# Performance work log

Measured on AMD Instinct MI355X. Metric: run time of the kernel, lower is better.

The kernel has to match this reference:

```python
import jax, jax.numpy as jnp
import numpy as np

K = 3  # kernel_size

def setup_inputs() -> dict:
    key = jax.random.key(0)
    ks = jax.random.split(key, 7)
    B, C, H, W = 4, 128, 128, 128
    MID = int(C * 0.2)  # 25
    return {
        "x":  jax.random.normal(ks[0], (B, C, H, W), dtype=jnp.float32),
        "Ws": jax.random.normal(ks[1], (K * K, C), dtype=jnp.float32) * 0.1,
        "bs": jax.random.normal(ks[2], (K * K,), dtype=jnp.float32) * 0.1,
        "W1": jax.random.normal(ks[3], (MID, C), dtype=jnp.float32) * 0.1,
        "b1": jax.random.normal(ks[4], (MID,), dtype=jnp.float32) * 0.1,
        "W2": jax.random.normal(ks[5], (C * K * K, MID), dtype=jnp.float32) * 0.1,
        "b2": jax.random.normal(ks[6], (C * K * K,), dtype=jnp.float32) * 0.1,
    }

def reference(x, Ws, bs, W1, b1, W2, b2):
    b, c, h, w = x.shape
    k = K
    # channel branch: global avg pool -> 1x1 conv -> relu -> 1x1 conv -> sigmoid
    xm = x.mean(axis=(2, 3))                                   # [b, c]
    hid = jax.nn.relu(xm @ W1.T + b1)                          # [b, mid]
    channel_filter = jax.nn.sigmoid(hid @ W2.T + b2)           # [b, c*k*k]
    channel_filter = channel_filter.reshape(b, c, k * k, 1, 1)
    # spatial branch: 1x1 conv C -> k*k, sigmoid
    spatial_filter = jax.nn.sigmoid(
        jnp.einsum('bchw,oc->bohw', x, Ws) + bs[None, :, None, None]
    ).reshape(b, 1, k * k, h, w)
    filt = spatial_filter * channel_filter                     # [b, c, k*k, h, w]
    # unfold (k=3, pad=1, stride=1, dilation=1): stack 9 shifted views
    xp = jnp.pad(x, ((0, 0), (0, 0), (1, 1), (1, 1)))
    patches = jnp.stack(
        [xp[:, :, i:i + h, j:j + w] for i in range(k) for j in range(k)],
        axis=2,
    )  # [b, c, k*k, h, w] — matches nn.Unfold's (c, k*k) ordering
    return (patches * filt).sum(axis=2)                        # [b, c, h, w]
```

## Files before the change

kernel.cpp:

```cpp
#include <hip/hip_runtime.h>

#define B 4
#define C 128
#define H 128
#define W 128
#define HW (H * W)
#define KK 9
#define MID 25

#define WS_XM 0
#define WS_CH 1024
#define WS_S  8192

__global__ __launch_bounds__(256) void k_mean(
    const float* __restrict__ x, float* __restrict__ xm)
{
    const int c = blockIdx.x, b = blockIdx.y;
    const float4* plane = (const float4*)(x + ((size_t)b * C + c) * HW);
    float s = 0.0f;
#pragma unroll
    for (int i = 0; i < 16; ++i) {
        float4 v = plane[i * 256 + threadIdx.x];
        s += (v.x + v.y) + (v.z + v.w);
    }
#pragma unroll
    for (int off = 32; off > 0; off >>= 1) s += __shfl_down(s, off, 64);
    __shared__ float red[4];
    if ((threadIdx.x & 63) == 0) red[threadIdx.x >> 6] = s;
    __syncthreads();
    if (threadIdx.x == 0)
        xm[b * C + c] = ((red[0] + red[1]) + (red[2] + red[3])) * (1.0f / HW);
}

__global__ __launch_bounds__(256) void k_spatial(
    const float* __restrict__ x, const float* __restrict__ Ws,
    const float* __restrict__ bs, float* __restrict__ S)
{
    const int lane = threadIdx.x & 63;
    const int wave = threadIdx.x >> 6;
    const int b = blockIdx.y;
    const int p = blockIdx.x * 64 + lane;
    const float* xb = x + (size_t)b * C * HW + p;

    float acc[KK];
#pragma unroll
    for (int k = 0; k < KK; ++k) acc[k] = (wave == 0) ? bs[k] : 0.0f;

    const int cbase = wave * 32;
#pragma unroll
    for (int i = 0; i < 32; ++i) {
        const int c = cbase + i;
        float v = xb[(size_t)c * HW];
#pragma unroll
        for (int k = 0; k < KK; ++k)
            acc[k] = fmaf(v, Ws[k * C + c], acc[k]);
    }

    __shared__ float red[3 * KK * 64];
    if (wave > 0) {
#pragma unroll
        for (int k = 0; k < KK; ++k)
            red[((wave - 1) * KK + k) * 64 + lane] = acc[k];
    }
    __syncthreads();
    if (wave == 0) {
#pragma unroll
        for (int k = 0; k < KK; ++k) {
            float a = acc[k] + red[(0 * KK + k) * 64 + lane]
                             + red[(1 * KK + k) * 64 + lane]
                             + red[(2 * KK + k) * 64 + lane];
            S[((size_t)(b * KK + k)) * HW + p] = 1.0f / (1.0f + __expf(-a));
        }
    }
}

__global__ __launch_bounds__(512) void k_mlp(
    const float* __restrict__ xm, const float* __restrict__ W1,
    const float* __restrict__ b1, const float* __restrict__ W2,
    const float* __restrict__ b2, float* __restrict__ ch)
{
    __shared__ float xmean[B * C];
    __shared__ float hid[B * MID];
    const int tid = threadIdx.x;

    if (tid < B * C) xmean[tid] = xm[tid];
    __syncthreads();

    if (tid < B * MID) {
        const int b = tid / MID, m = tid % MID;
        float a = b1[m];
        for (int c = 0; c < C; ++c)
            a = fmaf(xmean[b * C + c], W1[m * C + c], a);
        hid[tid] = fmaxf(a, 0.0f);
    }
    __syncthreads();

    for (int idx = tid; idx < B * C * KK; idx += 512) {
        const int b = idx / (C * KK);
        const int o = idx % (C * KK);
        float a = b2[o];
#pragma unroll
        for (int m = 0; m < MID; ++m)
            a = fmaf(hid[b * MID + m], W2[o * MID + m], a);
        ch[idx] = 1.0f / (1.0f + __expf(-a));
    }
}

__global__ __launch_bounds__(256) void k_conv(
    const float* __restrict__ x, const float* __restrict__ S,
    const float* __restrict__ ch, float* __restrict__ out)
{
    const int tid = threadIdx.x;
    const int b = blockIdx.y;
    const int p = blockIdx.x * 256 + tid;
    const int h = p / W, w = p % W;

    float sv[KK];
    int off[KK];
    const float* Sb = S + (size_t)b * KK * HW + p;
#pragma unroll
    for (int k = 0; k < KK; ++k) {
        const int di = k / 3 - 1, dj = k % 3 - 1;
        const int hh = h + di, ww = w + dj;
        const bool valid = (hh >= 0) & (hh < H) & (ww >= 0) & (ww < W);
        const int hc = min(max(hh, 0), H - 1);
        const int wc = min(max(ww, 0), W - 1);
        off[k] = hc * W + wc;
        sv[k] = valid ? Sb[(size_t)k * HW] : 0.0f;
    }

    const int c0 = blockIdx.z * (C / 8);
    const float* xb = x + (size_t)b * C * HW;
    const float* chb = ch + b * C * KK;
    float* ob = out + (size_t)b * C * HW;

#pragma unroll 4
    for (int c = c0; c < c0 + C / 8; ++c) {
        const float* xc = xb + (size_t)c * HW;
        float acc = 0.0f;
#pragma unroll
        for (int k = 0; k < KK; ++k) {
            acc = fmaf(xc[off[k]], sv[k] * chb[c * KK + k], acc);
        }
        ob[(size_t)c * HW + p] = acc;
    }
}

extern "C" void kernel_launch(void* const* d_in, const int* in_sizes, int n_in,
                              void* d_out, int out_size, void* d_ws, size_t ws_size,
                              hipStream_t stream) {
    (void)in_sizes; (void)n_in; (void)out_size; (void)ws_size;
    const float* x  = (const float*)d_in[0];
    const float* Ws = (const float*)d_in[1];
    const float* bs = (const float*)d_in[2];
    const float* W1 = (const float*)d_in[3];
    const float* b1 = (const float*)d_in[4];
    const float* W2 = (const float*)d_in[5];
    const float* b2 = (const float*)d_in[6];
    float* out = (float*)d_out;
    float* ws  = (float*)d_ws;

    float* xm = ws + WS_XM;
    float* ch = ws + WS_CH;
    float* S  = ws + WS_S;

    k_mean<<<dim3(C, B), 256, 0, stream>>>(x, xm);
    k_spatial<<<dim3(HW / 64, B), 256, 0, stream>>>(x, Ws, bs, S);
    k_mlp<<<1, 512, 0, stream>>>(xm, W1, b1, W2, b2, ch);
    k_conv<<<dim3(HW / 256, B, 8), 256, 0, stream>>>(x, S, ch, out);
}
```

Baseline: 134.8 us.

## Fuse mean and spatial kernels, parallelize MLP, vectorize conv to four pixels per thread

Merges the mean-pool and spatial-filter kernels into one launch by giving them different block ranges, which removes one launch and lets both read x concurrently. The channel MLP is split across 18 blocks instead of running in one block. Each conv thread now computes four adjacent pixels with float4 loads and reuses each row between the shifted taps, so fewer scalar gathers are issued. The channel split doubles to 16 groups to keep enough blocks in flight. Every MLP block recomputes the hidden layer, and the float4 path assumes W is a multiple of 4.

```diff
diff --git a/kernel.cpp b/kernel.cpp
--- a/kernel.cpp
+++ b/kernel.cpp
@@ -8,37 +8,40 @@
 #define KK 9
 #define MID 25
 
+#define SPATIAL_BLKS (HW / 64)
+
 #define WS_XM 0
 #define WS_CH 1024
 #define WS_S  8192
 
-__global__ __launch_bounds__(256) void k_mean(
-    const float* __restrict__ x, float* __restrict__ xm)
+__global__ __launch_bounds__(256) void k_ms(
+    const float* __restrict__ x, const float* __restrict__ Ws,
+    const float* __restrict__ bs, float* __restrict__ xm,
+    float* __restrict__ S)
 {
-    const int c = blockIdx.x, b = blockIdx.y;
-    const float4* plane = (const float4*)(x + ((size_t)b * C + c) * HW);
-    float s = 0.0f;
+    __shared__ float red[3 * KK * 64];
+    const int b = blockIdx.y;
+
+    if (blockIdx.x >= SPATIAL_BLKS) {
+        const int c = blockIdx.x - SPATIAL_BLKS;
+        const float4* plane = (const float4*)(x + ((size_t)b * C + c) * HW);
+        float s = 0.0f;
 #pragma unroll
-    for (int i = 0; i < 16; ++i) {
-        float4 v = plane[i * 256 + threadIdx.x];
-        s += (v.x + v.y) + (v.z + v.w);
+        for (int i = 0; i < 16; ++i) {
+            float4 v = plane[i * 256 + threadIdx.x];
+            s += (v.x + v.y) + (v.z + v.w);
+        }
+#pragma unroll
+        for (int off = 32; off > 0; off >>= 1) s += __shfl_down(s, off, 64);
+        if ((threadIdx.x & 63) == 0) red[threadIdx.x >> 6] = s;
+        __syncthreads();
+        if (threadIdx.x == 0)
+            xm[b * C + c] = ((red[0] + red[1]) + (red[2] + red[3])) * (1.0f / HW);
+        return;
     }
-#pragma unroll
-    for (int off = 32; off > 0; off >>= 1) s += __shfl_down(s, off, 64);
-    __shared__ float red[4];
-    if ((threadIdx.x & 63) == 0) red[threadIdx.x >> 6] = s;
-    __syncthreads();
-    if (threadIdx.x == 0)
-        xm[b * C + c] = ((red[0] + red[1]) + (red[2] + red[3])) * (1.0f / HW);
-}
 
-__global__ __launch_bounds__(256) void k_spatial(
-    const float* __restrict__ x, const float* __restrict__ Ws,
-    const float* __restrict__ bs, float* __restrict__ S)
-{
     const int lane = threadIdx.x & 63;
     const int wave = threadIdx.x >> 6;
-    const int b = blockIdx.y;
     const int p = blockIdx.x * 64 + lane;
     const float* xb = x + (size_t)b * C * HW + p;
 
@@ -56,7 +59,6 @@
             acc[k] = fmaf(v, Ws[k * C + c], acc[k]);
     }
 
-    __shared__ float red[3 * KK * 64];
     if (wave > 0) {
 #pragma unroll
         for (int k = 0; k < KK; ++k)
@@ -74,7 +76,7 @@
     }
 }
 
-__global__ __launch_bounds__(512) void k_mlp(
+__global__ __launch_bounds__(256) void k_mlp(
     const float* __restrict__ xm, const float* __restrict__ W1,
     const float* __restrict__ b1, const float* __restrict__ W2,
     const float* __restrict__ b2, float* __restrict__ ch)
@@ -83,27 +85,27 @@
     __shared__ float hid[B * MID];
     const int tid = threadIdx.x;
 
-    if (tid < B * C) xmean[tid] = xm[tid];
+    for (int i = tid; i < B * C; i += 256) xmean[i] = xm[i];
     __syncthreads();
 
     if (tid < B * MID) {
         const int b = tid / MID, m = tid % MID;
         float a = b1[m];
+#pragma unroll 8
         for (int c = 0; c < C; ++c)
             a = fmaf(xmean[b * C + c], W1[m * C + c], a);
         hid[tid] = fmaxf(a, 0.0f);
     }
     __syncthreads();
 
-    for (int idx = tid; idx < B * C * KK; idx += 512) {
-        const int b = idx / (C * KK);
-        const int o = idx % (C * KK);
-        float a = b2[o];
+    const int idx = blockIdx.x * 256 + tid;
+    const int b = idx / (C * KK);
+    const int o = idx % (C * KK);
+    float a = b2[o];
 #pragma unroll
-        for (int m = 0; m < MID; ++m)
-            a = fmaf(hid[b * MID + m], W2[o * MID + m], a);
-        ch[idx] = 1.0f / (1.0f + __expf(-a));
-    }
+    for (int m = 0; m < MID; ++m)
+        a = fmaf(hid[b * MID + m], W2[o * MID + m], a);
+    ch[idx] = 1.0f / (1.0f + __expf(-a));
 }
 
 __global__ __launch_bounds__(256) void k_conv(
@@ -112,37 +114,59 @@
 {
     const int tid = threadIdx.x;
     const int b = blockIdx.y;
-    const int p = blockIdx.x * 256 + tid;
-    const int h = p / W, w = p % W;
+    const int p0 = (blockIdx.x * 256 + tid) * 4;
+    const int h = p0 >> 7;
+    const int w0 = p0 & (W - 1);
 
-    float sv[KK];
-    int off[KK];
-    const float* Sb = S + (size_t)b * KK * HW + p;
+    float4 sv[KK];
+    const float* Sb = S + (size_t)b * KK * HW + p0;
 #pragma unroll
     for (int k = 0; k < KK; ++k) {
         const int di = k / 3 - 1, dj = k % 3 - 1;
-        const int hh = h + di, ww = w + dj;
-        const bool valid = (hh >= 0) & (hh < H) & (ww >= 0) & (ww < W);
-        const int hc = min(max(hh, 0), H - 1);
-        const int wc = min(max(ww, 0), W - 1);
-        off[k] = hc * W + wc;
-        sv[k] = valid ? Sb[(size_t)k * HW] : 0.0f;
+        const int hh = h + di;
+        float4 s4 = *(const float4*)(Sb + (size_t)k * HW);
+        if (hh < 0 || hh >= H) s4 = make_float4(0.f, 0.f, 0.f, 0.f);
+        if (dj == -1 && w0 == 0)     s4.x = 0.f;
+        if (dj == +1 && w0 == W - 4) s4.w = 0.f;
+        sv[k] = s4;
     }
 
-    const int c0 = blockIdx.z * (C / 8);
+    const int r0 = max(h - 1, 0), r2 = min(h + 1, H - 1);
+    const int rowoff[3] = { r0 * W + w0, h * W + w0, r2 * W + w0 };
+    const int loff = (w0 > 0) ? -1 : 0;
+    const int roff = (w0 < W - 4) ? 4 : 0;
+
+    const int c0 = blockIdx.z * (C / 16);
     const float* xb = x + (size_t)b * C * HW;
     const float* chb = ch + b * C * KK;
-    float* ob = out + (size_t)b * C * HW;
+    float* ob = out + (size_t)b * C * HW + p0;
 
-#pragma unroll 4
-    for (int c = c0; c < c0 + C / 8; ++c) {
+    for (int c = c0; c < c0 + C / 16; ++c) {
         const float* xc = xb + (size_t)c * HW;
-        float acc = 0.0f;
+        float4 Cx[3];
+        float  Lw[3], Rx[3];
+#pragma unroll
+        for (int r = 0; r < 3; ++r) {
+            const float* bp = xc + rowoff[r];
+            Cx[r] = *(const float4*)bp;
+            Lw[r] = bp[loff];
+            Rx[r] = bp[roff];
+        }
+        float4 a = make_float4(0.f, 0.f, 0.f, 0.f);
 #pragma unroll
         for (int k = 0; k < KK; ++k) {
-            acc = fmaf(xc[off[k]], sv[k] * chb[c * KK + k], acc);
+            const int r = k / 3, dj = k % 3 - 1;
+            float4 t;
+            if (dj == -1)     t = make_float4(Lw[r], Cx[r].x, Cx[r].y, Cx[r].z);
+            else if (dj == 0) t = Cx[r];
+            else              t = make_float4(Cx[r].y, Cx[r].z, Cx[r].w, Rx[r]);
+            const float cf = chb[c * KK + k];
+            a.x = fmaf(t.x, sv[k].x * cf, a.x);
+            a.y = fmaf(t.y, sv[k].y * cf, a.y);
+            a.z = fmaf(t.z, sv[k].z * cf, a.z);
+            a.w = fmaf(t.w, sv[k].w * cf, a.w);
         }
-        ob[(size_t)c * HW + p] = acc;
+        *(float4*)(ob + (size_t)c * HW) = a;
     }
 }
 
@@ -164,8 +188,7 @@
     float* ch = ws + WS_CH;
     float* S  = ws + WS_S;
 
-    k_mean<<<dim3(C, B), 256, 0, stream>>>(x, xm);
-    k_spatial<<<dim3(HW / 64, B), 256, 0, stream>>>(x, Ws, bs, S);
-    k_mlp<<<1, 512, 0, stream>>>(xm, W1, b1, W2, b2, ch);
-    k_conv<<<dim3(HW / 256, B, 8), 256, 0, stream>>>(x, S, ch, out);
+    k_ms<<<dim3(SPATIAL_BLKS + C, B), 256, 0, stream>>>(x, Ws, bs, xm, S);
+    k_mlp<<<18, 256, 0, stream>>>(xm, W1, b1, W2, b2, ch);
+    k_conv<<<dim3(HW / 1024, B, 16), 256, 0, stream>>>(x, S, ch, out);
 }
```

Result: faster. 127.0 us (-5.8%).
